# Performance work log

Measured on AMD Instinct MI355X. Metric: run time of the kernel, lower is better.

The kernel has to match this reference:

```python
import jax, jax.numpy as jnp
import numpy as np

B, IN, H, HEADS, W, P = 512, 512, 1024, 16, 32, 64
EPS = 1e-5

def _pe(w, p, dtype=jnp.float32):
    # sinusoidal positional encoding over the attention window, [w, p]
    pos = jnp.arange(w, dtype=dtype)[:, None]
    div = jnp.exp(-jnp.arange(0, p, 2, dtype=dtype) * (np.log(10000.0) / p))
    ang = pos * div[None, :]
    pe = jnp.zeros((w, p), dtype)
    pe = pe.at[:, 0::2].set(jnp.sin(ang))
    pe = pe.at[:, 1::2].set(jnp.cos(ang))
    return pe

def _bn(x, g, b, m, v):
    # BatchNorm1d in eval mode (running stats)
    return (x - m) * (g / jnp.sqrt(v + EPS)) + b

def setup_inputs():
    key = jax.random.key(0)
    ks = iter(jax.random.split(key, 40))
    s = 1.0 / np.sqrt(H)  # init_parameters('pytorch_default'): U(-1/sqrt(H), 1/sqrt(H))
    u = lambda shape: jax.random.uniform(next(ks), shape, jnp.float32, -s, s)
    rn = lambda shape: jax.random.normal(next(ks), shape, jnp.float32)
    return {
        "x": rn((B, IN)),
        "prev_hidden": rn((B, H)),
        "prev_cell": rn((B, H)),
        "past_cells": rn((W, B, H)),
        "W_ih": u((4 * H, IN)), "b_ih": u((4 * H,)),
        "W_hh": u((4 * H, H)),
        "W_q": u((H, IN + H)), "b_q": u((H,)),
        "W_ac": u((4 * H, H)), "b_ac": u((4 * H,)),
        "Wq_a": u((H, H)), "bq_a": u((H,)),
        "Wk_a": u((H, H + P)), "bk_a": u((H,)),
        "Wv_a": u((H, H + P)), "bv_a": u((H,)),
        "Wo_a": u((H, H)), "bo_a": u((H,)),
        "bn_attn_gamma": u((H,)), "bn_attn_beta": u((H,)),
        "bn_attn_mean": jnp.zeros((H,)), "bn_attn_var": jnp.ones((H,)),
        "bn_post_gamma": u((H,)), "bn_post_beta": u((H,)),
        "bn_post_mean": jnp.zeros((H,)), "bn_post_var": jnp.ones((H,)),
    }

def reference(x, prev_hidden, prev_cell, past_cells, W_ih, b_ih, W_hh, W_q, b_q, W_ac, b_ac, Wq_a, bq_a, Wk_a, bk_a, Wv_a, bv_a, Wo_a, bo_a, bn_attn_gamma, bn_attn_beta, bn_attn_mean, bn_attn_var, bn_post_gamma, bn_post_beta, bn_post_mean, bn_post_var):
    dk = H // HEADS
    # Q = elu(Wq * concat(x, h) + b)
    q = jax.nn.elu(jnp.concatenate([x, prev_hidden], -1) @ W_q.T + b_q)      # [B,H]
    # K = V = window of past cell states (+ positional encoding on features)
    vals = jnp.transpose(past_cells, (1, 0, 2))                              # [B,W,H]
    pe = jnp.broadcast_to(_pe(W, P)[None], (vals.shape[0], W, P))
    kv = jnp.concatenate([vals, pe], -1)                                     # [B,W,H+P]
    Q = (q @ Wq_a.T + bq_a).reshape(-1, HEADS, dk)                           # [B,h,dk]
    K = jax.nn.elu(kv @ Wk_a.T + bk_a).reshape(-1, W, HEADS, dk)             # activation_on_keys_and_values
    V = jax.nn.elu(kv @ Wv_a.T + bv_a).reshape(-1, W, HEADS, dk)
    scores = jnp.einsum('bhd,bwhd->bhw', Q, K) / np.sqrt(dk)
    ctx = jnp.einsum('bhw,bwhd->bhd', jax.nn.softmax(scores, -1), V).reshape(-1, H)
    attn = jax.nn.elu(ctx @ Wo_a.T + bo_a)                                   # [B,H]
    attn = _bn(attn, bn_attn_gamma, bn_attn_beta, bn_attn_mean, bn_attn_var)
    # 'residual' mode: Wx*x + Wh*h + Wa*a + b  (note: original returns pre-BN value)
    pre = x @ W_ih.T + b_ih + prev_hidden @ W_hh.T + attn @ W_ac.T + b_ac    # [B,4H]
    iv = jnp.tanh(pre[:, :H])
    gates = jax.nn.sigmoid(pre[:, H:])
    f, i, o = gates[:, :H], gates[:, H:2 * H], gates[:, 2 * H:]
    cell = iv * i + prev_cell * f
    hidden = _bn(o * jax.nn.elu(cell), bn_post_gamma, bn_post_beta, bn_post_mean, bn_post_var)
    return hidden
```

## Files before the change

### kernel.cpp

```cpp
#include <hip/hip_runtime.h>
#include <hip/hip_bf16.h>

typedef __attribute__((ext_vector_type(8))) short s16x8;
typedef __attribute__((ext_vector_type(8))) unsigned short u16x8;
typedef __attribute__((ext_vector_type(4))) float f32x4;

__device__ __forceinline__ float bf2f(unsigned short u) {
  union { unsigned int i; float f; } v; v.i = ((unsigned int)u) << 16; return v.f;
}
__device__ __forceinline__ unsigned short f2bf(float f) {
  union { float f; unsigned int i; } v; v.f = f;
  unsigned int u = v.i;
  unsigned int r = (u + 0x7fffu + ((u >> 16) & 1u)) >> 16;
  return (unsigned short)r;
}
__device__ __forceinline__ float eluf(float x) { return x > 0.f ? x : __expf(x) - 1.f; }
__device__ __forceinline__ float sigf(float x) { return 1.f / (1.f + __expf(-x)); }
__device__ __forceinline__ float tanhfast(float x) {
  float ax = fminf(fabsf(x), 15.f);
  float e2 = __expf(2.f * ax);
  float t = (e2 - 1.f) / (e2 + 1.f);
  return x < 0.f ? -t : t;
}

__device__ __forceinline__ void gl_lds16(const unsigned short* g, unsigned short* l) {
  __builtin_amdgcn_global_load_lds(
      (const __attribute__((address_space(1))) void*)g,
      (__attribute__((address_space(3))) void*)l, 16, 0, 0);
}

template<int N> __device__ __forceinline__ void waitv() {
  if constexpr (N == 0) asm volatile("s_waitcnt vmcnt(0)" ::: "memory");
  else if constexpr (N == 3) asm volatile("s_waitcnt vmcnt(3)" ::: "memory");
  else if constexpr (N == 4) asm volatile("s_waitcnt vmcnt(4)" ::: "memory");
  else if constexpr (N == 6) asm volatile("s_waitcnt vmcnt(6)" ::: "memory");
  else if constexpr (N == 8) asm volatile("s_waitcnt vmcnt(8)" ::: "memory");
}
__device__ __forceinline__ void sbar() {
  __builtin_amdgcn_sched_barrier(0);
  __builtin_amdgcn_s_barrier();
  __builtin_amdgcn_sched_barrier(0);
}

struct CP {
  const float *pcs, *W_ih, *W_hh, *W_ac, *W_q, *Wq_a, *Wo_a, *Wk_a, *Wv_a, *x, *ph;
  const float *b_ih, *b_ac, *bk, *bv;
  const float *g1, *be1, *m1, *v1, *g2, *be2, *m2, *v2;
  unsigned short *A_pc, *W6, *Wq, *Wqa, *Woa, *Wkv, *A6;
  float *peb, *bias6, *s1, *t1, *s2, *t2;
};

__global__ __launch_bounds__(256)
void cast_all(CP p) {
  int c = blockIdx.x * 256 + threadIdx.x;
  const float* src; unsigned short* dst; int row, col, ldd;
  if (c < 2097152) {
    row = c >> 7; col = (c & 127) << 3;
    src = p.pcs + (size_t)row * 1024 + col; dst = p.A_pc; ldd = 1024;
  } else if (c < 3407872) {
    int i = c - 2097152; int orow = i / 320; col = (i - orow * 320) << 3;
    dst = p.W6; ldd = 2560;
    src = (col < 512)  ? p.W_ih + (size_t)orow * 512 + col
        : (col < 1536) ? p.W_hh + (size_t)orow * 1024 + (col - 512)
                       : p.W_ac + (size_t)orow * 1024 + (col - 1536);
    row = (orow & 1023) * 4 + (orow >> 10);
  } else if (c < 3604480) {
    int i = c - 3407872; row = i / 192; col = (i - row * 192) << 3;
    src = p.W_q + (size_t)row * 1536 + col; dst = p.Wq; ldd = 1536;
  } else if (c < 3735552) {
    int i = c - 3604480; row = i >> 7; col = (i & 127) << 3;
    src = p.Wq_a + (size_t)row * 1024 + col; dst = p.Wqa; ldd = 1024;
  } else if (c < 3866624) {
    int i = c - 3735552; row = i >> 7; col = (i & 127) << 3;
    src = p.Wo_a + (size_t)row * 1024 + col; dst = p.Woa; ldd = 1024;
  } else if (c < 4128768) {
    int i = c - 3866624; row = i >> 7; col = (i & 127) << 3;
    src = (row < 1024) ? p.Wk_a + (size_t)row * 1088 + col
                       : p.Wv_a + (size_t)(row - 1024) * 1088 + col;
    dst = p.Wkv; ldd = 1024;
  } else if (c < 4227072) {
    int i = c - 4128768; row = i / 192; col = (i - row * 192) << 3;
    src = (col < 512) ? p.x + (size_t)row * 512 + col
                      : p.ph + (size_t)row * 1024 + (col - 512);
    dst = p.A6; ldd = 2560;
  } else if (c < 4292608) {
    int idx = c - 4227072;
    int w = idx >> 11, n = idx & 2047;
    const float* Wrow =
        ((n < 1024) ? (p.Wk_a + (size_t)n * 1088)
                    : (p.Wv_a + (size_t)(n - 1024) * 1088)) + 1024;
    float accv = (n < 1024) ? p.bk[n] : p.bv[n - 1024];
    const float c0 = 0.14391157f;
#pragma unroll
    for (int j = 0; j < 32; ++j) {
      float ang = (float)w * __expf(-(2.f * j) * c0);
      accv += __sinf(ang) * Wrow[2 * j] + __cosf(ang) * Wrow[2 * j + 1];
    }
    p.peb[idx] = accv;
    return;
  } else {
    int i = c - 4292608;
    if (i < 4096) p.bias6[(i & 1023) * 4 + (i >> 10)] = p.b_ih[i] + p.b_ac[i];
    if (i < 1024) {
      float sa = p.g1[i] * rsqrtf(p.v1[i] + 1e-5f);
      p.s1[i] = sa; p.t1[i] = p.be1[i] - p.m1[i] * sa;
      float sp = p.g2[i] * rsqrtf(p.v2[i] + 1e-5f);
      p.s2[i] = sp; p.t2[i] = p.be2[i] - p.m2[i] * sp;
    }
    return;
  }
  f32x4 v0 = *(const f32x4*)src;
  f32x4 v1 = *(const f32x4*)(src + 4);
  u16x8 r;
  r[0] = f2bf(v0.x); r[1] = f2bf(v0.y); r[2] = f2bf(v0.z); r[3] = f2bf(v0.w);
  r[4] = f2bf(v1.x); r[5] = f2bf(v1.y); r[6] = f2bf(v1.z); r[7] = f2bf(v1.w);
  int sc = col ^ ((row & 7) << 3);
  *(u16x8*)(dst + (size_t)row * ldd + sc) = r;
}

struct GP2 {
  const unsigned short* A; long lda;
  const unsigned short* B; long ldb;
  const float* bias;
  const float* bnS; const float* bnT;
  const float* pcell;
  float* of; unsigned short* ob;
  int N, K;
};

template<int BM, int BN, int EPI, int ACT>
__global__ __launch_bounds__(256)
void sgemm(GP2 p) {
  constexpr int LA = (BM * 8) / 256, LB = (BN * 8) / 256, L = LA + LB;
  __shared__ unsigned short sA[3][BM * 64];
  __shared__ unsigned short sB[3][BN * 64];
  const int tid = threadIdx.x, lane = tid & 63, wid = tid >> 6;
  const int col0 = blockIdx.x * BN, row0 = blockIdx.y * BM;
  constexpr int WRS = BM / 2, WCS = BN / 2;
  constexpr int MI = WRS / 16, NI = WCS / 16;
  const int wr = (wid >> 1) * WRS, wc = (wid & 1) * WCS;
  const int g = lane >> 4, lr = lane & 15;
  f32x4 acc[MI][NI] = {};

  auto stage = [&](int buf, int kb) {
#pragma unroll
    for (int i = 0; i < LA; ++i) {
      int chunk = i * 256 + tid;
      int r = chunk >> 3, c8 = chunk & 7;
      gl_lds16(p.A + (size_t)(row0 + r) * p.lda + kb + c8 * 8, &sA[buf][chunk * 8]);
    }
#pragma unroll
    for (int i = 0; i < LB; ++i) {
      int chunk = i * 256 + tid;
      int r = chunk >> 3, c8 = chunk & 7;
      gl_lds16(p.B + (size_t)(col0 + r) * p.ldb + kb + c8 * 8, &sB[buf][chunk * 8]);
    }
  };
  auto compute = [&](int buf) {
#pragma unroll
    for (int kk = 0; kk < 64; kk += 32) {
      s16x8 af[MI], bf_[NI];
#pragma unroll
      for (int i = 0; i < MI; ++i) {
        int ar = wr + i * 16 + lr;
        int sl = ((kk >> 3) + g) ^ (ar & 7);
        af[i] = *(const s16x8*)(&sA[buf][(ar * 8 + sl) * 8]);
      }
#pragma unroll
      for (int i = 0; i < NI; ++i) {
        int br = wc + i * 16 + lr;
        int sl = ((kk >> 3) + g) ^ (br & 7);
        bf_[i] = *(const s16x8*)(&sB[buf][(br * 8 + sl) * 8]);
      }
#pragma unroll
      for (int mi = 0; mi < MI; ++mi)
#pragma unroll
        for (int ni = 0; ni < NI; ++ni)
          acc[mi][ni] = __builtin_amdgcn_mfma_f32_16x16x32_bf16(
              af[mi], bf_[ni], acc[mi][ni], 0, 0, 0);
    }
  };

  const int nt = p.K >> 6;
  stage(0, 0);
  stage(1, 64);
  int bufc = 0;
  for (int t = 0; t < nt; ++t) {
    if (t + 2 < nt) {
      stage(bufc >= 1 ? bufc - 1 : bufc + 2, (t + 2) << 6);
      waitv<2 * L>();
    } else if (t + 1 < nt) {
      waitv<L>();
    } else {
      waitv<0>();
    }
    sbar();
    compute(bufc);
    sbar();
    bufc = bufc < 2 ? bufc + 1 : 0;
  }

#pragma unroll
  for (int mi = 0; mi < MI; ++mi) {
#pragma unroll
    for (int ni = 0; ni < NI; ++ni) {
#pragma unroll
      for (int rg = 0; rg < 4; ++rg) {
        int rr = row0 + wr + mi * 16 + g * 4 + rg;
        int cc = col0 + wc + ni * 16 + lr;
        float v = acc[mi][ni][rg] + p.bias[cc];
        if constexpr (ACT) v = eluf(v);
        if constexpr (EPI == 0) {
          p.of[(size_t)rr * p.N + cc] = v;
        } else if constexpr (EPI == 1) {
          p.ob[(size_t)rr * p.N + (cc ^ ((rr & 7) << 3))] = f2bf(v);
        } else if constexpr (EPI == 3) {
          v = v * p.bnS[cc] + p.bnT[cc];
          p.ob[(size_t)rr * 2560 + ((1536 + cc) ^ ((rr & 7) << 3))] = f2bf(v);
        } else {
          int base = lane & ~3;
          float g0 = __shfl(v, base);
          float g1 = __shfl(v, base | 1);
          float g2v = __shfl(v, base | 2);
          float g3 = __shfl(v, base | 3);
          if ((lane & 3) == 0) {
            int j = cc >> 2;
            float iv = tanhfast(g0);
            float fg = sigf(g1);
            float ig = sigf(g2v);
            float og = sigf(g3);
            float cell = iv * ig + p.pcell[(size_t)rr * 1024 + j] * fg;
            float ec = cell > 0.f ? cell : __expf(cell) - 1.f;
            p.of[(size_t)rr * 1024 + j] = (og * ec) * p.bnS[j] + p.bnT[j];
          }
        }
      }
    }
  }
}

__global__ __launch_bounds__(256)
void gkv_attn(const unsigned short* __restrict__ A_pc,
              const unsigned short* __restrict__ Wkv,
              const float* __restrict__ peb,
              const float* __restrict__ Qf,
              unsigned short* __restrict__ ctx) {
  __shared__ unsigned short smem[2 * 128 * 64];
  __shared__ float prs[4][32];
  __shared__ float qs[4][64];
  unsigned short* sA = smem;
  unsigned short* sB = smem + 128 * 64;

  int id = blockIdx.x;
  int nid = (id & 7) * 256 + (id >> 3);
  const int h = nid & 15, bg = nid >> 4;
  const int b0 = bg * 4;

  const int tid = threadIdx.x, lane = tid & 63, wid = tid >> 6;
  const int wr = (wid >> 1) * 64, wc = (wid & 1) * 64;
  const int g = lane >> 4, lr = lane & 15;
  f32x4 acc[4][4] = {};

  for (int kb = 0; kb < 1024; kb += 64) {
    __syncthreads();
#pragma unroll
    for (int ps = 0; ps < 4; ++ps) {
      int chunk = ps * 256 + tid;
      int r = chunk >> 3, c8 = chunk & 7;
      int w = r >> 2;
      int srow = w * 512 + b0 + (r & 3);
      int xf = (r & 7) ^ (srow & 7);
      gl_lds16(A_pc + (size_t)srow * 1024 + kb + ((c8 ^ xf) << 3), &sA[chunk * 8]);
    }
#pragma unroll
    for (int ps = 0; ps < 4; ++ps) {
      int chunk = ps * 256 + tid;
      int r = chunk >> 3, c8 = chunk & 7;
      int n = h * 64 + r + (r >= 64 ? 960 : 0);
      gl_lds16(Wkv + (size_t)n * 1024 + kb + (c8 << 3), &sB[chunk * 8]);
    }
    __syncthreads();
#pragma unroll
    for (int kk = 0; kk < 64; kk += 32) {
      s16x8 af[4], bf_[4];
#pragma unroll
      for (int i = 0; i < 4; ++i) {
        int ar = wr + i * 16 + lr;
        int sl = ((kk >> 3) + g) ^ (ar & 7);
        af[i] = *(const s16x8*)(&sA[(ar * 8 + sl) * 8]);
        int br = wc + i * 16 + lr;
        int sl2 = ((kk >> 3) + g) ^ (br & 7);
        bf_[i] = *(const s16x8*)(&sB[(br * 8 + sl2) * 8]);
      }
#pragma unroll
      for (int mi = 0; mi < 4; ++mi)
#pragma unroll
        for (int ni = 0; ni < 4; ++ni)
          acc[mi][ni] = __builtin_amdgcn_mfma_f32_16x16x32_bf16(
              af[mi], bf_[ni], acc[mi][ni], 0, 0, 0);
    }
  }
  __syncthreads();

  unsigned short (*kv)[128] = (unsigned short(*)[128])smem;
#pragma unroll
  for (int mi = 0; mi < 4; ++mi) {
#pragma unroll
    for (int ni = 0; ni < 4; ++ni) {
#pragma unroll
      for (int rg = 0; rg < 4; ++rg) {
        int rr = wr + mi * 16 + g * 4 + rg;
        int cc = wc + ni * 16 + lr;
        int w = rr >> 2;
        int gcol = h * 64 + cc + (cc >= 64 ? 960 : 0);
        float v = acc[mi][ni][rg] + peb[w * 2048 + gcol];
        v = v > 0.f ? v : __expf(v) - 1.f;
        kv[rr][cc ^ ((rr & 7) << 3)] = f2bf(v);
      }
    }
  }
  qs[wid][lane] = Qf[(size_t)(b0 + wid) * 1024 + h * 64 + lane];
  __syncthreads();

  const int wv = wid;
  const int w = lane & 31, half = lane >> 5;
  float s = 0.f;
  {
    int r = w * 4 + wv;
    int swz = r & 7;
#pragma unroll
    for (int jj = 0; jj < 4; ++jj) {
      u16x8 kx = *(const u16x8*)(&kv[r][((half * 4 + jj) ^ swz) << 3]);
#pragma unroll
      for (int e = 0; e < 8; ++e)
        s += qs[wv][half * 32 + jj * 8 + e] * bf2f(kx[e]);
    }
  }
  s += __shfl_xor(s, 32);
  s *= 0.125f;
  float mx = s;
#pragma unroll
  for (int off = 16; off; off >>= 1) mx = fmaxf(mx, __shfl_xor(mx, off));
  float e = __expf(s - mx);
  float sum = e;
#pragma unroll
  for (int off = 16; off; off >>= 1) sum += __shfl_xor(sum, off);
  if (lane < 32) prs[wv][lane] = e / sum;

  float c = 0.f;
  const int d = lane;
#pragma unroll 8
  for (int w2 = 0; w2 < 32; ++w2) {
    int r = w2 * 4 + wv;
    c += prs[wv][w2] * bf2f(kv[r][(64 + d) ^ ((r & 7) << 3)]);
  }
  int b = b0 + wv;
  ctx[(size_t)b * 1024 + ((h * 64 + d) ^ ((b & 7) << 3))] = f2bf(c);
}

extern "C" void kernel_launch(void* const* d_in, const int* in_sizes, int n_in,
                              void* d_out, int out_size, void* d_ws, size_t ws_size,
                              hipStream_t stream) {
  (void)in_sizes; (void)n_in; (void)out_size; (void)ws_size;
  const float* x     = (const float*)d_in[0];
  const float* ph    = (const float*)d_in[1];
  const float* pcell = (const float*)d_in[2];
  const float* pcs   = (const float*)d_in[3];
  const float* W_ih  = (const float*)d_in[4];
  const float* b_ih  = (const float*)d_in[5];
  const float* W_hh  = (const float*)d_in[6];
  const float* W_q   = (const float*)d_in[7];
  const float* b_q   = (const float*)d_in[8];
  const float* W_ac  = (const float*)d_in[9];
  const float* b_ac  = (const float*)d_in[10];
  const float* Wq_a  = (const float*)d_in[11];
  const float* bq_a  = (const float*)d_in[12];
  const float* Wk_a  = (const float*)d_in[13];
  const float* bk_a  = (const float*)d_in[14];
  const float* Wv_a  = (const float*)d_in[15];
  const float* bv_a  = (const float*)d_in[16];
  const float* Wo_a  = (const float*)d_in[17];
  const float* bo_a  = (const float*)d_in[18];

  char* wp = (char*)d_ws;
  auto alloc = [&](size_t bytes) {
    char* r = wp; wp += (bytes + 255) & ~(size_t)255; return r;
  };
  unsigned short* A_pc  = (unsigned short*)alloc((size_t)16384 * 1024 * 2);
  unsigned short* W6    = (unsigned short*)alloc((size_t)4096 * 2560 * 2);
  unsigned short* Wq    = (unsigned short*)alloc((size_t)1024 * 1536 * 2);
  unsigned short* Wqa   = (unsigned short*)alloc((size_t)1024 * 1024 * 2);
  unsigned short* Woa   = (unsigned short*)alloc((size_t)1024 * 1024 * 2);
  unsigned short* Wkv   = (unsigned short*)alloc((size_t)2048 * 1024 * 2);
  unsigned short* A6    = (unsigned short*)alloc((size_t)512 * 2560 * 2);
  unsigned short* q_bf  = (unsigned short*)alloc((size_t)512 * 1024 * 2);
  float*          Qf    = (float*)alloc((size_t)512 * 1024 * 4);
  unsigned short* ctxbf = (unsigned short*)alloc((size_t)512 * 1024 * 2);
  float*          peb   = (float*)alloc((size_t)32 * 2048 * 4);
  float*          bias6 = (float*)alloc((size_t)4096 * 4);
  float*          s1    = (float*)alloc((size_t)1024 * 4);
  float*          t1    = (float*)alloc((size_t)1024 * 4);
  float*          s2    = (float*)alloc((size_t)1024 * 4);
  float*          t2    = (float*)alloc((size_t)1024 * 4);

  {
    CP cp = {};
    cp.pcs = pcs; cp.W_ih = W_ih; cp.W_hh = W_hh; cp.W_ac = W_ac; cp.W_q = W_q;
    cp.Wq_a = Wq_a; cp.Wo_a = Wo_a; cp.Wk_a = Wk_a; cp.Wv_a = Wv_a;
    cp.x = x; cp.ph = ph;
    cp.b_ih = b_ih; cp.b_ac = b_ac; cp.bk = bk_a; cp.bv = bv_a;
    cp.g1 = (const float*)d_in[19]; cp.be1 = (const float*)d_in[20];
    cp.m1 = (const float*)d_in[21]; cp.v1 = (const float*)d_in[22];
    cp.g2 = (const float*)d_in[23]; cp.be2 = (const float*)d_in[24];
    cp.m2 = (const float*)d_in[25]; cp.v2 = (const float*)d_in[26];
    cp.A_pc = A_pc; cp.W6 = W6; cp.Wq = Wq; cp.Wqa = Wqa; cp.Woa = Woa;
    cp.Wkv = Wkv; cp.A6 = A6;
    cp.peb = peb; cp.bias6 = bias6; cp.s1 = s1; cp.t1 = t1; cp.s2 = s2; cp.t2 = t2;
    cast_all<<<16784, 256, 0, stream>>>(cp);
  }

  {
    GP2 p = {};
    p.A = A6; p.lda = 2560; p.B = Wq; p.ldb = 1536;
    p.bias = b_q; p.ob = q_bf; p.N = 1024; p.K = 1536;
    sgemm<32, 64, 1, 1><<<dim3(16, 16), 256, 0, stream>>>(p);
  }
  {
    GP2 p = {};
    p.A = q_bf; p.lda = 1024; p.B = Wqa; p.ldb = 1024;
    p.bias = bq_a; p.of = Qf; p.N = 1024; p.K = 1024;
    sgemm<32, 64, 0, 0><<<dim3(16, 16), 256, 0, stream>>>(p);
  }
  gkv_attn<<<2048, 256, 0, stream>>>(A_pc, Wkv, peb, Qf, ctxbf);
  {
    GP2 p = {};
    p.A = ctxbf; p.lda = 1024; p.B = Woa; p.ldb = 1024;
    p.bias = bo_a; p.bnS = s1; p.bnT = t1; p.ob = A6; p.N = 1024; p.K = 1024;
    sgemm<32, 64, 3, 1><<<dim3(16, 16), 256, 0, stream>>>(p);
  }
  {
    GP2 p = {};
    p.A = A6; p.lda = 2560; p.B = W6; p.ldb = 2560;
    p.bias = bias6; p.bnS = s2; p.bnT = t2; p.pcell = pcell;
    p.of = (float*)d_out; p.N = 4096; p.K = 2560;
    sgemm<64, 64, 4, 0><<<dim3(64, 8), 256, 0, stream>>>(p);
  }
}
```

Measured before the change: 375.5 us.

## Process two attention heads per block in fused KV-projection attention kernel

Each gkv_attn block now computes K/V projections for two heads instead of one, widening the B tile to 256 columns and doubling per-wave accumulators. The A tile of past cells is loaded once and reused across both heads, halving A-operand global traffic and the grid size. The cost is higher register use (32 accumulator tiles, launch bounds set to 2 blocks/CU), larger LDS, and each wave doing two softmax/context passes.

```diff
diff --git a/kernel.cpp b/kernel.cpp
--- a/kernel.cpp
+++ b/kernel.cpp
@@ -239,27 +239,28 @@
   }
 }
 
-__global__ __launch_bounds__(256)
+__global__ __launch_bounds__(256, 2)
 void gkv_attn(const unsigned short* __restrict__ A_pc,
               const unsigned short* __restrict__ Wkv,
               const float* __restrict__ peb,
               const float* __restrict__ Qf,
               unsigned short* __restrict__ ctx) {
-  __shared__ unsigned short smem[2 * 128 * 64];
-  __shared__ float prs[4][32];
-  __shared__ float qs[4][64];
+  __shared__ unsigned short smem[128 * 256];
+  __shared__ float prs[8][32];
+  __shared__ float qs[4][128];
   unsigned short* sA = smem;
   unsigned short* sB = smem + 128 * 64;
 
   int id = blockIdx.x;
-  int nid = (id & 7) * 256 + (id >> 3);
-  const int h = nid & 15, bg = nid >> 4;
+  int nid = (id & 7) * 128 + (id >> 3);
+  const int hp = nid & 7, bg = nid >> 3;
+  const int h_base = hp * 2;
   const int b0 = bg * 4;
 
   const int tid = threadIdx.x, lane = tid & 63, wid = tid >> 6;
-  const int wr = (wid >> 1) * 64, wc = (wid & 1) * 64;
+  const int wr = (wid >> 1) * 64, wc = (wid & 1) * 128;
   const int g = lane >> 4, lr = lane & 15;
-  f32x4 acc[4][4] = {};
+  f32x4 acc[4][8] = {};
 
   for (int kb = 0; kb < 1024; kb += 64) {
     __syncthreads();
@@ -273,21 +274,25 @@
       gl_lds16(A_pc + (size_t)srow * 1024 + kb + ((c8 ^ xf) << 3), &sA[chunk * 8]);
     }
 #pragma unroll
-    for (int ps = 0; ps < 4; ++ps) {
+    for (int ps = 0; ps < 8; ++ps) {
       int chunk = ps * 256 + tid;
       int r = chunk >> 3, c8 = chunk & 7;
-      int n = h * 64 + r + (r >= 64 ? 960 : 0);
+      int c7 = r & 127, h2 = r >> 7;
+      int n = (h_base + h2) * 64 + (c7 & 63) + ((c7 >> 6) << 10);
       gl_lds16(Wkv + (size_t)n * 1024 + kb + (c8 << 3), &sB[chunk * 8]);
     }
     __syncthreads();
 #pragma unroll
     for (int kk = 0; kk < 64; kk += 32) {
-      s16x8 af[4], bf_[4];
+      s16x8 af[4], bf_[8];
 #pragma unroll
       for (int i = 0; i < 4; ++i) {
         int ar = wr + i * 16 + lr;
         int sl = ((kk >> 3) + g) ^ (ar & 7);
         af[i] = *(const s16x8*)(&sA[(ar * 8 + sl) * 8]);
+      }
+#pragma unroll
+      for (int i = 0; i < 8; ++i) {
         int br = wc + i * 16 + lr;
         int sl2 = ((kk >> 3) + g) ^ (br & 7);
         bf_[i] = *(const s16x8*)(&sB[(br * 8 + sl2) * 8]);
@@ -295,67 +300,81 @@
 #pragma unroll
       for (int mi = 0; mi < 4; ++mi)
 #pragma unroll
-        for (int ni = 0; ni < 4; ++ni)
+        for (int ni = 0; ni < 8; ++ni)
           acc[mi][ni] = __builtin_amdgcn_mfma_f32_16x16x32_bf16(
               af[mi], bf_[ni], acc[mi][ni], 0, 0, 0);
     }
   }
   __syncthreads();
 
-  unsigned short (*kv)[128] = (unsigned short(*)[128])smem;
+  unsigned short (*kv)[256] = (unsigned short(*)[256])smem;
 #pragma unroll
   for (int mi = 0; mi < 4; ++mi) {
 #pragma unroll
-    for (int ni = 0; ni < 4; ++ni) {
+    for (int ni = 0; ni < 8; ++ni) {
 #pragma unroll
       for (int rg = 0; rg < 4; ++rg) {
         int rr = wr + mi * 16 + g * 4 + rg;
         int cc = wc + ni * 16 + lr;
         int w = rr >> 2;
-        int gcol = h * 64 + cc + (cc >= 64 ? 960 : 0);
+        int c7 = cc & 127, h2 = cc >> 7;
+        int gcol = (h_base + h2) * 64 + (c7 & 63) + ((c7 >> 6) << 10);
         float v = acc[mi][ni][rg] + peb[w * 2048 + gcol];
         v = v > 0.f ? v : __expf(v) - 1.f;
         kv[rr][cc ^ ((rr & 7) << 3)] = f2bf(v);
       }
     }
   }
-  qs[wid][lane] = Qf[(size_t)(b0 + wid) * 1024 + h * 64 + lane];
+  {
+    int i0 = tid;
+    qs[i0 >> 7][i0 & 127] =
+        Qf[(size_t)(b0 + (i0 >> 7)) * 1024 + h_base * 64 + (i0 & 127)];
+    int i1 = tid + 256;
+    qs[i1 >> 7][i1 & 127] =
+        Qf[(size_t)(b0 + (i1 >> 7)) * 1024 + h_base * 64 + (i1 & 127)];
+  }
   __syncthreads();
 
-  const int wv = wid;
   const int w = lane & 31, half = lane >> 5;
-  float s = 0.f;
-  {
-    int r = w * 4 + wv;
+#pragma unroll
+  for (int pi = 0; pi < 2; ++pi) {
+    int p = wid * 2 + pi;
+    int bb = p & 3, h2 = p >> 2;
+    int r = w * 4 + bb;
     int swz = r & 7;
+    float s = 0.f;
 #pragma unroll
     for (int jj = 0; jj < 4; ++jj) {
-      u16x8 kx = *(const u16x8*)(&kv[r][((half * 4 + jj) ^ swz) << 3]);
+      int c8idx = h2 * 16 + half * 4 + jj;
+      u16x8 kx = *(const u16x8*)(&kv[r][(c8idx ^ swz) << 3]);
 #pragma unroll
       for (int e = 0; e < 8; ++e)
-        s += qs[wv][half * 32 + jj * 8 + e] * bf2f(kx[e]);
-    }
-  }
-  s += __shfl_xor(s, 32);
-  s *= 0.125f;
-  float mx = s;
-#pragma unroll
-  for (int off = 16; off; off >>= 1) mx = fmaxf(mx, __shfl_xor(mx, off));
-  float e = __expf(s - mx);
-  float sum = e;
-#pragma unroll
-  for (int off = 16; off; off >>= 1) sum += __shfl_xor(sum, off);
-  if (lane < 32) prs[wv][lane] = e / sum;
-
-  float c = 0.f;
-  const int d = lane;
+        s += qs[bb][h2 * 64 + half * 32 + jj * 8 + e] * bf2f(kx[e]);
+    }
+    s += __shfl_xor(s, 32);
+    s *= 0.125f;
+    float mx = s;
+#pragma unroll
+    for (int off = 16; off; off >>= 1) mx = fmaxf(mx, __shfl_xor(mx, off));
+    float e = __expf(s - mx);
+    float sum = e;
+#pragma unroll
+    for (int off = 16; off; off >>= 1) sum += __shfl_xor(sum, off);
+    if (lane < 32) prs[p][lane] = e / sum;
+    __builtin_amdgcn_wave_barrier();
+
+    float c = 0.f;
+    const int d = lane;
+    int vcol = h2 * 128 + 64 + d;
 #pragma unroll 8
-  for (int w2 = 0; w2 < 32; ++w2) {
-    int r = w2 * 4 + wv;
-    c += prs[wv][w2] * bf2f(kv[r][(64 + d) ^ ((r & 7) << 3)]);
-  }
-  int b = b0 + wv;
-  ctx[(size_t)b * 1024 + ((h * 64 + d) ^ ((b & 7) << 3))] = f2bf(c);
+    for (int w2 = 0; w2 < 32; ++w2) {
+      int r2 = w2 * 4 + bb;
+      c += prs[p][w2] * bf2f(kv[r2][vcol ^ ((r2 & 7) << 3)]);
+    }
+    int b = b0 + bb;
+    int ocol = (h_base + h2) * 64 + d;
+    ctx[(size_t)b * 1024 + (ocol ^ ((b & 7) << 3))] = f2bf(c);
+  }
 }
 
 extern "C" void kernel_launch(void* const* d_in, const int* in_sizes, int n_in,
@@ -431,7 +450,7 @@
     p.bias = bq_a; p.of = Qf; p.N = 1024; p.K = 1024;
     sgemm<32, 64, 0, 0><<<dim3(16, 16), 256, 0, stream>>>(p);
   }
-  gkv_attn<<<2048, 256, 0, stream>>>(A_pc, Wkv, peb, Qf, ctxbf);
+  gkv_attn<<<1024, 256, 0, stream>>>(A_pc, Wkv, peb, Qf, ctxbf);
   {
     GP2 p = {};
     p.A = ctxbf; p.lda = 1024; p.B = Woa; p.ldb = 1024;
```

Measured after the change: 351.4 us. 1.07x faster.
